# Optimization experiments

Measured on AMD Instinct MI355X. Metric: run time of the kernel, lower is better.

The kernel has to match this reference:

```python
import jax, jax.numpy as jnp
import numpy as np

B, D, G, F, A = 262144, 128, 8, 80, 18  # batch, obs dim, n_games, n_features, max_actions


def setup_inputs() -> dict:
    key = jax.random.key(0)
    ks = jax.random.split(key, 10)
    s1 = 1.0 / np.sqrt(D)
    s2 = 1.0 / np.sqrt(F)
    state = jax.random.normal(ks[0], (B, D), dtype=jnp.float32)
    idx = jnp.sort(jax.random.randint(ks[1], (B,), 0, G, dtype=jnp.int32))
    W1 = jax.random.normal(ks[2], (G, F, D), dtype=jnp.float32) * s1
    b1 = jax.random.normal(ks[3], (G, F), dtype=jnp.float32) * s1
    W2 = jax.random.normal(ks[4], (F, F), dtype=jnp.float32) * s2
    b2 = jax.random.normal(ks[5], (F,), dtype=jnp.float32) * s2
    W3 = jax.random.normal(ks[6], (F, F), dtype=jnp.float32) * s2
    b3 = jax.random.normal(ks[7], (F,), dtype=jnp.float32) * s2
    W4 = jax.random.normal(ks[8], (G, A, F), dtype=jnp.float32) * s2
    b4 = jax.random.normal(ks[9], (G, A), dtype=jnp.float32) * s2
    return {"state": state, "idx": idx, "W1": W1, "b1": b1, "W2": W2, "b2": b2,
            "W3": W3, "b3": b3, "W4": W4, "b4": b4}


def reference(state, idx, W1, b1, W2, b2, W3, b3, W4, b4):
    state = state.astype(jnp.float32)
    n_games = W1.shape[0]
    # Routed first layer: each sample goes through its game's Linear(D->F).
    # Loop is over the small fixed set of games; batch dim stays vectorized.
    h1 = jnp.zeros((state.shape[0], W1.shape[1]), dtype=state.dtype)
    for g in range(n_games):
        hg = state @ W1[g].T + b1[g]  # [B, F]
        h1 = h1 + jnp.where((idx == g)[:, None], hg, jnp.zeros((), state.dtype))
    h1 = jax.nn.relu(h1)
    # Shared MLP (features == 'relu')
    h = jax.nn.relu(h1 @ W2.T + b2)
    h = jax.nn.relu(h @ W3.T + b3)
    # All per-game heads, stacked: q[b, g, a]
    q = jnp.einsum('bf,gaf->bga', h, W4) + b4  # [B, G, A]
    # Gather the head matching each sample's game (action=None branch)
    q_idx = jnp.take_along_axis(q, idx[:, None, None].astype(jnp.int32), axis=1)  # [B,1,A]
    return jnp.squeeze(q_idx, axis=1)  # [B, A]
```

## Files before the change

kernel.cpp:

```cpp
#include <hip/hip_runtime.h>


#define B_TOT   262144
#define DDIM    128
#define NGAMES  8
#define FDIM    80
#define ADIM    18
#define ROWS_W  32
#define MT      128
#define SH      104

#define W1SW    0
#define W2SW    81920
#define W3SW    89600
#define W4SW    97280
#define WTOT    121856

#define LW1     0
#define LW2     10240
#define LW3     17920
#define LHB     25600
#define LDS_SH  38912

typedef __attribute__((ext_vector_type(8))) short short8;
typedef __attribute__((ext_vector_type(4))) float floatx4;

static __device__ __forceinline__ unsigned short f2bf(float f) {
  union { float f; unsigned u; } v; v.f = f;
  unsigned r = v.u + 0x7fffu + ((v.u >> 16) & 1u);
  return (unsigned short)(r >> 16);
}

__global__ void convert_weights(const float* __restrict__ W1, const float* __restrict__ W2,
                                const float* __restrict__ W3, const float* __restrict__ W4,
                                unsigned short* __restrict__ ws) {
  int t = blockIdx.x * 256 + threadIdx.x;
  if (t >= WTOT) return;
  int chunk = t >> 9, r = t & 511;
  int lane = r >> 3, j = r & 7;
  int l16 = lane & 15, quad = lane >> 4;
  float val;
  if (chunk < 160) {
    int g = chunk / 20, rem = chunk % 20, ks = rem / 5, ct = rem % 5;
    int n = ct * 16 + l16, k = ks * 32 + quad * 8 + j;
    val = W1[(g * FDIM + n) * DDIM + k];
  } else if (chunk < 175) {
    int c = chunk - 160, ks = c / 5, ct = c % 5;
    int n = ct * 16 + l16, k = ks * 32 + quad * 8 + j;
    val = (k < FDIM) ? W2[n * FDIM + k] : 0.f;
  } else if (chunk < 190) {
    int c = chunk - 175, ks = c / 5, ct = c % 5;
    int n = ct * 16 + l16, k = ks * 32 + quad * 8 + j;
    val = (k < FDIM) ? W3[n * FDIM + k] : 0.f;
  } else {
    int c = chunk - 190, g = c / 6, rem = c % 6, ks = rem >> 1, ct = rem & 1;
    int n = ct * 16 + l16, k = ks * 32 + quad * 8 + j;
    val = (n < ADIM && k < FDIM) ? W4[(g * ADIM + n) * FDIM + k] : 0.f;
  }
  ws[t] = f2bf(val);
}

static __device__ __forceinline__ short8 ld_frag8_f32(const float* p) {
  floatx4 a = *(const floatx4*)p;
  floatx4 b = *(const floatx4*)(p + 4);
  short8 r;
  r[0] = (short)f2bf(a[0]); r[1] = (short)f2bf(a[1]);
  r[2] = (short)f2bf(a[2]); r[3] = (short)f2bf(a[3]);
  r[4] = (short)f2bf(b[0]); r[5] = (short)f2bf(b[1]);
  r[6] = (short)f2bf(b[2]); r[7] = (short)f2bf(b[3]);
  return r;
}

static __device__ __forceinline__ void mlp_layer_inplace(
    unsigned short* hbuf,
    const unsigned short* lw,
    const float* __restrict__ bias,
    int lane, int l16, int quad)
{
  short8 a[2][3];
#pragma unroll
  for (int s = 0; s < 2; ++s)
#pragma unroll
    for (int ks = 0; ks < 3; ++ks)
      a[s][ks] = *(const short8*)(hbuf + (s * 16 + l16) * SH + ks * 32 + quad * 8);

  floatx4 acc[2][5];
#pragma unroll
  for (int s = 0; s < 2; ++s)
#pragma unroll
    for (int ct = 0; ct < 5; ++ct) acc[s][ct] = (floatx4){0.f, 0.f, 0.f, 0.f};
#pragma unroll
  for (int ks = 0; ks < 3; ++ks)
#pragma unroll
    for (int ct = 0; ct < 5; ++ct) {
      short8 bf = *(const short8*)(lw + (ks * 5 + ct) * 512 + lane * 8);
      acc[0][ct] = __builtin_amdgcn_mfma_f32_16x16x32_bf16(a[0][ks], bf, acc[0][ct], 0, 0, 0);
      acc[1][ct] = __builtin_amdgcn_mfma_f32_16x16x32_bf16(a[1][ks], bf, acc[1][ct], 0, 0, 0);
    }
#pragma unroll
  for (int s = 0; s < 2; ++s)
#pragma unroll
    for (int ct = 0; ct < 5; ++ct) {
      int col = ct * 16 + l16;
      float bv = bias[col];
#pragma unroll
      for (int r = 0; r < 4; ++r) {
        int row = s * 16 + quad * 4 + r;
        hbuf[row * SH + col] = f2bf(fmaxf(acc[s][ct][r] + bv, 0.f));
      }
    }
}

__global__ __launch_bounds__(256, 2) void gym_fused(
    const float* __restrict__ state, const int* __restrict__ idx,
    const unsigned short* __restrict__ wsw,
    const float* __restrict__ b1, const float* __restrict__ b2,
    const float* __restrict__ b3, const float* __restrict__ b4,
    float* __restrict__ out)
{
  __shared__ __align__(16) unsigned short smem[LDS_SH];

  const int tid  = threadIdx.x;
  const int lane = tid & 63;
  const int wv   = tid >> 6;
  const int l16  = lane & 15;
  const int quad = lane >> 4;
  unsigned short* hbuf = smem + LHB + wv * (ROWS_W * SH);
  const size_t blk_row0 = (size_t)blockIdx.x * MT;
  const size_t row0 = blk_row0 + wv * ROWS_W;
  const short8 zero8 = {0, 0, 0, 0, 0, 0, 0, 0};

  int idxr[2][4];
#pragma unroll
  for (int s = 0; s < 2; ++s)
#pragma unroll
    for (int r = 0; r < 4; ++r) idxr[s][r] = idx[row0 + s * 16 + quad * 4 + r];
  const int g_lo = idx[blk_row0];
  const int g_hi = idx[blk_row0 + MT - 1];

  {
    const short8* src = (const short8*)(wsw + W2SW);
    short8* dst = (short8*)(smem + LW2);
#pragma unroll
    for (int i = 0; i < 8; ++i) {
      int t = i * 256 + tid;
      if (t < 1920) dst[t] = src[t];
    }
  }

  {
    int r = lane >> 1, cc = lane & 1;
    *(short8*)(hbuf + r * SH + 80 + cc * 8) = zero8;
  }

  short8 afrag[2][4];
#pragma unroll
  for (int s = 0; s < 2; ++s) {
    const float* sp = state + (row0 + s * 16 + l16) * DDIM + quad * 8;
#pragma unroll
    for (int ks = 0; ks < 4; ++ks)
      afrag[s][ks] = ld_frag8_f32(sp + ks * 32);
  }

  for (int g = g_lo; g <= g_hi; ++g) {
    {
      const short8* src = (const short8*)(wsw + W1SW + g * (20 * 512));
      short8* dst = (short8*)(smem + LW1);
#pragma unroll
      for (int i = 0; i < 5; ++i)
        dst[i * 256 + tid] = src[i * 256 + tid];
    }
    __syncthreads();

    {
      floatx4 acc[2][5];
#pragma unroll
      for (int s = 0; s < 2; ++s)
#pragma unroll
        for (int ct = 0; ct < 5; ++ct) acc[s][ct] = (floatx4){0.f, 0.f, 0.f, 0.f};
#pragma unroll
      for (int ks = 0; ks < 4; ++ks)
#pragma unroll
        for (int ct = 0; ct < 5; ++ct) {
          short8 bf = *(const short8*)(smem + LW1 + (ks * 5 + ct) * 512 + lane * 8);
          acc[0][ct] = __builtin_amdgcn_mfma_f32_16x16x32_bf16(afrag[0][ks], bf, acc[0][ct], 0, 0, 0);
          acc[1][ct] = __builtin_amdgcn_mfma_f32_16x16x32_bf16(afrag[1][ks], bf, acc[1][ct], 0, 0, 0);
        }
#pragma unroll
      for (int s = 0; s < 2; ++s)
#pragma unroll
        for (int ct = 0; ct < 5; ++ct) {
          int col = ct * 16 + l16;
          float bv = b1[g * FDIM + col];
#pragma unroll
          for (int r = 0; r < 4; ++r) {
            int row = s * 16 + quad * 4 + r;
            hbuf[row * SH + col] = f2bf(fmaxf(acc[s][ct][r] + bv, 0.f));
          }
        }
    }

    mlp_layer_inplace(hbuf, smem + LW2, b2, lane, l16, quad);
    mlp_layer_inplace(hbuf, smem + LW3, b3, lane, l16, quad);

    {
      short8 a3[2][3];
#pragma unroll
      for (int s = 0; s < 2; ++s)
#pragma unroll
        for (int ks = 0; ks < 3; ++ks)
          a3[s][ks] = *(const short8*)(hbuf + (s * 16 + l16) * SH + ks * 32 + quad * 8);

      floatx4 acc[2][2];
#pragma unroll
      for (int s = 0; s < 2; ++s)
#pragma unroll
        for (int ct = 0; ct < 2; ++ct) acc[s][ct] = (floatx4){0.f, 0.f, 0.f, 0.f};
#pragma unroll
      for (int ks = 0; ks < 3; ++ks)
#pragma unroll
        for (int ct = 0; ct < 2; ++ct) {
          short8 bf = *(const short8*)(wsw + W4SW + (((g * 3 + ks) * 2) + ct) * 512 + lane * 8);
          acc[0][ct] = __builtin_amdgcn_mfma_f32_16x16x32_bf16(a3[0][ks], bf, acc[0][ct], 0, 0, 0);
          acc[1][ct] = __builtin_amdgcn_mfma_f32_16x16x32_bf16(a3[1][ks], bf, acc[1][ct], 0, 0, 0);
        }
#pragma unroll
      for (int s = 0; s < 2; ++s)
#pragma unroll
        for (int ct = 0; ct < 2; ++ct) {
          int col = ct * 16 + l16;
          if (col < ADIM) {
            float bv = b4[g * ADIM + col];
#pragma unroll
            for (int r = 0; r < 4; ++r) {
              if (idxr[s][r] == g)
                out[(row0 + s * 16 + quad * 4 + r) * ADIM + col] = acc[s][ct][r] + bv;
            }
          }
        }
    }

    if (g < g_hi) __syncthreads();
  }
}

extern "C" void kernel_launch(void* const* d_in, const int* in_sizes, int n_in,
                              void* d_out, int out_size, void* d_ws, size_t ws_size,
                              hipStream_t stream) {
  const float* state = (const float*)d_in[0];
  const int*   idx   = (const int*)d_in[1];
  const float* W1    = (const float*)d_in[2];
  const float* b1    = (const float*)d_in[3];
  const float* W2    = (const float*)d_in[4];
  const float* b2    = (const float*)d_in[5];
  const float* W3    = (const float*)d_in[6];
  const float* b3    = (const float*)d_in[7];
  const float* W4    = (const float*)d_in[8];
  const float* b4    = (const float*)d_in[9];
  float*       out   = (float*)d_out;
  unsigned short* wsw = (unsigned short*)d_ws;

  convert_weights<<<(WTOT + 255) / 256, 256, 0, stream>>>(W1, W2, W3, W4, wsw);
  gym_fused<<<B_TOT / MT, 256, 0, stream>>>(state, idx, wsw, b1, b2, b3, b4, out);
}
```

Measured before the change: 235.2 us.

## Make blocks persistent over four tiles with prefetched state and cached game weights

Each block now processes four consecutive 128-row tiles instead of one. The next tile's state rows are loaded into registers while the current tile computes. W1 is restaged into LDS only when the game changes. W4 fragments and biases are held in registers, and a masked template path handles tiles that span several games. The aim is to hide global-load latency and cut per-block weight staging and launch overhead, at the cost of more register pressure and a quarter as many blocks.

```diff
diff --git a/kernel.cpp b/kernel.cpp
--- a/kernel.cpp
+++ b/kernel.cpp
@@ -3,11 +3,12 @@
 
 #define B_TOT   262144
 #define DDIM    128
-#define NGAMES  8
 #define FDIM    80
 #define ADIM    18
 #define ROWS_W  32
 #define MT      128
+#define SPAN    512
+#define NITER   4
 #define SH      104
 
 #define W1SW    0
@@ -60,21 +61,37 @@
   ws[t] = f2bf(val);
 }
 
-static __device__ __forceinline__ short8 ld_frag8_f32(const float* p) {
-  floatx4 a = *(const floatx4*)p;
-  floatx4 b = *(const floatx4*)(p + 4);
-  short8 r;
-  r[0] = (short)f2bf(a[0]); r[1] = (short)f2bf(a[1]);
-  r[2] = (short)f2bf(a[2]); r[3] = (short)f2bf(a[3]);
-  r[4] = (short)f2bf(b[0]); r[5] = (short)f2bf(b[1]);
-  r[6] = (short)f2bf(b[2]); r[7] = (short)f2bf(b[3]);
-  return r;
+static __device__ __forceinline__ void stage_game(
+    int g, const unsigned short* __restrict__ wsw, unsigned short* smem,
+    const float* __restrict__ b1, const float* __restrict__ b4,
+    int tid, int lane, int l16,
+    short8 w4f[6], float b1v[5], float b4v[2])
+{
+  __syncthreads();
+  {
+    const short8* src = (const short8*)(wsw + W1SW + g * (20 * 512));
+    short8* dst = (short8*)(smem + LW1);
+#pragma unroll
+    for (int i = 0; i < 5; ++i)
+      dst[i * 256 + tid] = src[i * 256 + tid];
+  }
+  __syncthreads();
+#pragma unroll
+  for (int ks = 0; ks < 3; ++ks)
+#pragma unroll
+    for (int ct = 0; ct < 2; ++ct)
+      w4f[ks * 2 + ct] = *(const short8*)(wsw + W4SW + (((g * 3 + ks) * 2) + ct) * 512 + lane * 8);
+#pragma unroll
+  for (int ct = 0; ct < 5; ++ct) b1v[ct] = b1[g * FDIM + ct * 16 + l16];
+#pragma unroll
+  for (int ct = 0; ct < 2; ++ct) {
+    int col = ct * 16 + l16;
+    b4v[ct] = (col < ADIM) ? b4[g * ADIM + col] : 0.f;
+  }
 }
 
 static __device__ __forceinline__ void mlp_layer_inplace(
-    unsigned short* hbuf,
-    const unsigned short* lw,
-    const float* __restrict__ bias,
+    unsigned short* hbuf, const unsigned short* lw, const float bv[5],
     int lane, int l16, int quad)
 {
   short8 a[2][3];
@@ -102,13 +119,85 @@
 #pragma unroll
     for (int ct = 0; ct < 5; ++ct) {
       int col = ct * 16 + l16;
-      float bv = bias[col];
 #pragma unroll
       for (int r = 0; r < 4; ++r) {
         int row = s * 16 + quad * 4 + r;
-        hbuf[row * SH + col] = f2bf(fmaxf(acc[s][ct][r] + bv, 0.f));
-      }
-    }
+        hbuf[row * SH + col] = f2bf(fmaxf(acc[s][ct][r] + bv[ct], 0.f));
+      }
+    }
+}
+
+template<bool MASKED>
+static __device__ __forceinline__ void compute_tile(
+    unsigned short* smem, unsigned short* hbuf,
+    const short8 afrag[2][4], const short8 w4f[6],
+    const float b1v[5], const float b2v[5], const float b3v[5], const float b4v[2],
+    const int idxr[2][4], int g, size_t row0,
+    int lane, int l16, int quad, float* __restrict__ out)
+{
+  {
+    floatx4 acc[2][5];
+#pragma unroll
+    for (int s = 0; s < 2; ++s)
+#pragma unroll
+      for (int ct = 0; ct < 5; ++ct) acc[s][ct] = (floatx4){0.f, 0.f, 0.f, 0.f};
+#pragma unroll
+    for (int ks = 0; ks < 4; ++ks)
+#pragma unroll
+      for (int ct = 0; ct < 5; ++ct) {
+        short8 bf = *(const short8*)(smem + LW1 + (ks * 5 + ct) * 512 + lane * 8);
+        acc[0][ct] = __builtin_amdgcn_mfma_f32_16x16x32_bf16(afrag[0][ks], bf, acc[0][ct], 0, 0, 0);
+        acc[1][ct] = __builtin_amdgcn_mfma_f32_16x16x32_bf16(afrag[1][ks], bf, acc[1][ct], 0, 0, 0);
+      }
+#pragma unroll
+    for (int s = 0; s < 2; ++s)
+#pragma unroll
+      for (int ct = 0; ct < 5; ++ct) {
+        int col = ct * 16 + l16;
+#pragma unroll
+        for (int r = 0; r < 4; ++r) {
+          if (!MASKED || idxr[s][r] == g) {
+            int row = s * 16 + quad * 4 + r;
+            hbuf[row * SH + col] = f2bf(fmaxf(acc[s][ct][r] + b1v[ct], 0.f));
+          }
+        }
+      }
+  }
+  mlp_layer_inplace(hbuf, smem + LW2, b2v, lane, l16, quad);
+  mlp_layer_inplace(hbuf, smem + LW3, b3v, lane, l16, quad);
+  {
+    short8 a3[2][3];
+#pragma unroll
+    for (int s = 0; s < 2; ++s)
+#pragma unroll
+      for (int ks = 0; ks < 3; ++ks)
+        a3[s][ks] = *(const short8*)(hbuf + (s * 16 + l16) * SH + ks * 32 + quad * 8);
+    floatx4 acc[2][2];
+#pragma unroll
+    for (int s = 0; s < 2; ++s)
+#pragma unroll
+      for (int ct = 0; ct < 2; ++ct) acc[s][ct] = (floatx4){0.f, 0.f, 0.f, 0.f};
+#pragma unroll
+    for (int ks = 0; ks < 3; ++ks)
+#pragma unroll
+      for (int ct = 0; ct < 2; ++ct) {
+        acc[0][ct] = __builtin_amdgcn_mfma_f32_16x16x32_bf16(a3[0][ks], w4f[ks * 2 + ct], acc[0][ct], 0, 0, 0);
+        acc[1][ct] = __builtin_amdgcn_mfma_f32_16x16x32_bf16(a3[1][ks], w4f[ks * 2 + ct], acc[1][ct], 0, 0, 0);
+      }
+#pragma unroll
+    for (int s = 0; s < 2; ++s)
+#pragma unroll
+      for (int ct = 0; ct < 2; ++ct) {
+        int col = ct * 16 + l16;
+        if (col < ADIM) {
+#pragma unroll
+          for (int r = 0; r < 4; ++r) {
+            if (!MASKED || idxr[s][r] == g)
+              out[(row0 + s * 16 + quad * 4 + r) * ADIM + col] = acc[s][ct][r] + b4v[ct];
+          }
+        }
+      }
+  }
 }
 
 __global__ __launch_bounds__(256, 2) void gym_fused(
@@ -126,17 +215,8 @@
   const int l16  = lane & 15;
   const int quad = lane >> 4;
   unsigned short* hbuf = smem + LHB + wv * (ROWS_W * SH);
-  const size_t blk_row0 = (size_t)blockIdx.x * MT;
-  const size_t row0 = blk_row0 + wv * ROWS_W;
+  const size_t blk0 = (size_t)blockIdx.x * SPAN;
   const short8 zero8 = {0, 0, 0, 0, 0, 0, 0, 0};
-
-  int idxr[2][4];
-#pragma unroll
-  for (int s = 0; s < 2; ++s)
-#pragma unroll
-    for (int r = 0; r < 4; ++r) idxr[s][r] = idx[row0 + s * 16 + quad * 4 + r];
-  const int g_lo = idx[blk_row0];
-  const int g_hi = idx[blk_row0 + MT - 1];
 
   {
     const short8* src = (const short8*)(wsw + W2SW);
@@ -147,100 +227,100 @@
       if (t < 1920) dst[t] = src[t];
     }
   }
-
   {
     int r = lane >> 1, cc = lane & 1;
     *(short8*)(hbuf + r * SH + 80 + cc * 8) = zero8;
   }
+  float b2v[5], b3v[5];
+#pragma unroll
+  for (int ct = 0; ct < 5; ++ct) {
+    b2v[ct] = b2[ct * 16 + l16];
+    b3v[ct] = b3[ct * 16 + l16];
+  }
+  int curr_g = idx[blk0];
+  short8 w4f[6]; float b1v[5], b4v[2];
+  stage_game(curr_g, wsw, smem, b1, b4, tid, lane, l16, w4f, b1v, b4v);
 
   short8 afrag[2][4];
 #pragma unroll
   for (int s = 0; s < 2; ++s) {
-    const float* sp = state + (row0 + s * 16 + l16) * DDIM + quad * 8;
-#pragma unroll
-    for (int ks = 0; ks < 4; ++ks)
-      afrag[s][ks] = ld_frag8_f32(sp + ks * 32);
-  }
-
-  for (int g = g_lo; g <= g_hi; ++g) {
-    {
-      const short8* src = (const short8*)(wsw + W1SW + g * (20 * 512));
-      short8* dst = (short8*)(smem + LW1);
-#pragma unroll
-      for (int i = 0; i < 5; ++i)
-        dst[i * 256 + tid] = src[i * 256 + tid];
-    }
-    __syncthreads();
-
-    {
-      floatx4 acc[2][5];
+    const float* sp = state + (blk0 + wv * ROWS_W + s * 16 + l16) * DDIM + quad * 8;
+#pragma unroll
+    for (int ks = 0; ks < 4; ++ks) {
+      floatx4 va = *(const floatx4*)(sp + ks * 32);
+      floatx4 vb = *(const floatx4*)(sp + ks * 32 + 4);
+      short8 f;
+      f[0] = (short)f2bf(va[0]); f[1] = (short)f2bf(va[1]);
+      f[2] = (short)f2bf(va[2]); f[3] = (short)f2bf(va[3]);
+      f[4] = (short)f2bf(vb[0]); f[5] = (short)f2bf(vb[1]);
+      f[6] = (short)f2bf(vb[2]); f[7] = (short)f2bf(vb[3]);
+      afrag[s][ks] = f;
+    }
+  }
+  int tg_lo = idx[blk0];
+  int tg_hi = idx[blk0 + MT - 1];
+
+  for (int it = 0; it < NITER; ++it) {
+    const size_t trow0 = blk0 + (size_t)it * MT;
+    const size_t row0  = trow0 + wv * ROWS_W;
+
+    floatx4 fnext[16];
+    int ntg_lo = 0, ntg_hi = 0;
+    if (it + 1 < NITER) {
+      ntg_lo = idx[trow0 + MT];
+      ntg_hi = idx[trow0 + 2 * MT - 1];
+#pragma unroll
+      for (int s = 0; s < 2; ++s) {
+        const float* sp = state + (row0 + MT + s * 16 + l16) * DDIM + quad * 8;
+#pragma unroll
+        for (int ks = 0; ks < 4; ++ks) {
+          fnext[(s * 4 + ks) * 2]     = *(const floatx4*)(sp + ks * 32);
+          fnext[(s * 4 + ks) * 2 + 1] = *(const floatx4*)(sp + ks * 32 + 4);
+        }
+      }
+    }
+
+    if (tg_lo == tg_hi) {
+      if (tg_lo != curr_g) {
+        stage_game(tg_lo, wsw, smem, b1, b4, tid, lane, l16, w4f, b1v, b4v);
+        curr_g = tg_lo;
+      }
+      int dummy[2][4];
+      compute_tile<false>(smem, hbuf, afrag, w4f, b1v, b2v, b3v, b4v,
+                          dummy, curr_g, row0, lane, l16, quad, out);
+    } else {
+      int idxr[2][4];
 #pragma unroll
       for (int s = 0; s < 2; ++s)
 #pragma unroll
-        for (int ct = 0; ct < 5; ++ct) acc[s][ct] = (floatx4){0.f, 0.f, 0.f, 0.f};
-#pragma unroll
-      for (int ks = 0; ks < 4; ++ks)
-#pragma unroll
-        for (int ct = 0; ct < 5; ++ct) {
-          short8 bf = *(const short8*)(smem + LW1 + (ks * 5 + ct) * 512 + lane * 8);
-          acc[0][ct] = __builtin_amdgcn_mfma_f32_16x16x32_bf16(afrag[0][ks], bf, acc[0][ct], 0, 0, 0);
-          acc[1][ct] = __builtin_amdgcn_mfma_f32_16x16x32_bf16(afrag[1][ks], bf, acc[1][ct], 0, 0, 0);
-        }
+        for (int r = 0; r < 4; ++r) idxr[s][r] = idx[row0 + s * 16 + quad * 4 + r];
+      for (int g = tg_lo; g <= tg_hi; ++g) {
+        if (g != curr_g) {
+          stage_game(g, wsw, smem, b1, b4, tid, lane, l16, w4f, b1v, b4v);
+          curr_g = g;
+        }
+        compute_tile<true>(smem, hbuf, afrag, w4f, b1v, b2v, b3v, b4v,
+                           idxr, g, row0, lane, l16, quad, out);
+      }
+    }
+
+    if (it + 1 < NITER) {
 #pragma unroll
       for (int s = 0; s < 2; ++s)
 #pragma unroll
-        for (int ct = 0; ct < 5; ++ct) {
-          int col = ct * 16 + l16;
-          float bv = b1[g * FDIM + col];
-#pragma unroll
-          for (int r = 0; r < 4; ++r) {
-            int row = s * 16 + quad * 4 + r;
-            hbuf[row * SH + col] = f2bf(fmaxf(acc[s][ct][r] + bv, 0.f));
-          }
-        }
-    }
-
-    mlp_layer_inplace(hbuf, smem + LW2, b2, lane, l16, quad);
-    mlp_layer_inplace(hbuf, smem + LW3, b3, lane, l16, quad);
-
-    {
-      short8 a3[2][3];
-#pragma unroll
-      for (int s = 0; s < 2; ++s)
-#pragma unroll
-        for (int ks = 0; ks < 3; ++ks)
-          a3[s][ks] = *(const short8*)(hbuf + (s * 16 + l16) * SH + ks * 32 + quad * 8);
-
-      floatx4 acc[2][2];
-#pragma unroll
-      for (int s = 0; s < 2; ++s)
-#pragma unroll
-        for (int ct = 0; ct < 2; ++ct) acc[s][ct] = (floatx4){0.f, 0.f, 0.f, 0.f};
-#pragma unroll
-      for (int ks = 0; ks < 3; ++ks)
-#pragma unroll
-        for (int ct = 0; ct < 2; ++ct) {
-          short8 bf = *(const short8*)(wsw + W4SW + (((g * 3 + ks) * 2) + ct) * 512 + lane * 8);
-          acc[0][ct] = __builtin_amdgcn_mfma_f32_16x16x32_bf16(a3[0][ks], bf, acc[0][ct], 0, 0, 0);
-          acc[1][ct] = __builtin_amdgcn_mfma_f32_16x16x32_bf16(a3[1][ks], bf, acc[1][ct], 0, 0, 0);
-        }
-#pragma unroll
-      for (int s = 0; s < 2; ++s)
-#pragma unroll
-        for (int ct = 0; ct < 2; ++ct) {
-          int col = ct * 16 + l16;
-          if (col < ADIM) {
-            float bv = b4[g * ADIM + col];
-#pragma unroll
-            for (int r = 0; r < 4; ++r) {
-              if (idxr[s][r] == g)
-                out[(row0 + s * 16 + quad * 4 + r) * ADIM + col] = acc[s][ct][r] + bv;
-            }
-          }
-        }
-    }
-
-    if (g < g_hi) __syncthreads();
+        for (int ks = 0; ks < 4; ++ks) {
+          floatx4 va = fnext[(s * 4 + ks) * 2];
+          floatx4 vb = fnext[(s * 4 + ks) * 2 + 1];
+          short8 f;
+          f[0] = (short)f2bf(va[0]); f[1] = (short)f2bf(va[1]);
+          f[2] = (short)f2bf(va[2]); f[3] = (short)f2bf(va[3]);
+          f[4] = (short)f2bf(vb[0]); f[5] = (short)f2bf(vb[1]);
+          f[6] = (short)f2bf(vb[2]); f[7] = (short)f2bf(vb[3]);
+          afrag[s][ks] = f;
+        }
+      tg_lo = ntg_lo;
+      tg_hi = ntg_hi;
+    }
   }
 }
 
@@ -261,5 +341,5 @@
   unsigned short* wsw = (unsigned short*)d_ws;
 
   convert_weights<<<(WTOT + 255) / 256, 256, 0, stream>>>(W1, W2, W3, W4, wsw);
-  gym_fused<<<B_TOT / MT, 256, 0, stream>>>(state, idx, wsw, b1, b2, b3, b4, out);
-}
+  gym_fused<<<B_TOT / SPAN, 256, 0, stream>>>(state, idx, wsw, b1, b2, b3, b4, out);
+}
```

Measured after the change: 254.5 us. 8.2% more time.
